# Optimization experiments

Measured on AMD Instinct MI355X. Metric: run time of the kernel, lower is better.

The kernel has to match this reference:

```python
import jax, jax.numpy as jnp
import numpy as np

B, L, D = 2, 2048, 1024
H = 16
DH = D // H
FACTOR = 0.6
U = max(1, min(L, int(FACTOR * L)))  # 1228 selected queries


def setup_inputs() -> dict:
    key = jax.random.key(0)
    ks = jax.random.split(key, 9)
    s = 0.02
    return {
        "x": jax.random.normal(ks[0], (B, L, D), dtype=jnp.float32),
        "Wq": jax.random.normal(ks[1], (D, D), dtype=jnp.float32) * s,
        "bq": jnp.zeros((D,), dtype=jnp.float32),
        "Wk": jax.random.normal(ks[2], (D, D), dtype=jnp.float32) * s,
        "bk": jnp.zeros((D,), dtype=jnp.float32),
        "Wv": jax.random.normal(ks[3], (D, D), dtype=jnp.float32) * s,
        "bv": jnp.zeros((D,), dtype=jnp.float32),
        "Wo": jax.random.normal(ks[4], (D, D), dtype=jnp.float32) * s,
        "bo": jnp.zeros((D,), dtype=jnp.float32),
    }


def _split_heads(x):
    b, l, d = x.shape
    return x.reshape(b, l, H, DH).transpose(0, 2, 1, 3)  # [b,h,l,dh]


def reference(x, Wq, bq, Wk, bk, Wv, bv, Wo, bo):
    b, l, _ = x.shape
    scale = 1.0 / jnp.sqrt(jnp.asarray(DH, dtype=x.dtype))

    q = _split_heads(x @ Wq + bq)  # [b,h,l,dh]
    k = _split_heads(x @ Wk + bk)
    v = _split_heads(x @ Wv + bv)

    # full scores for sparsity heuristic
    scores = jnp.einsum("bhqd,bhkd->bhqk", q, k) * scale  # [b,h,l,l]
    sparsity = scores.max(axis=-1) - scores.mean(axis=-1)  # [b,h,l]

    _, top_idx = jax.lax.top_k(sparsity, U)  # [b,h,U]

    # gather selected queries, attend only on those rows
    q_sel = jnp.take_along_axis(q, top_idx[..., None], axis=2)  # [b,h,U,dh]
    scores_sel = jnp.einsum("bhud,bhkd->bhuk", q_sel, k) * scale  # [b,h,U,l]
    attn = jax.nn.softmax(scores_sel, axis=-1)
    out_sel = jnp.einsum("bhuk,bhkd->bhud", attn, v)  # [b,h,U,dh]

    # scatter back into zero-initialized output
    bi = jnp.arange(b)[:, None, None]
    hi = jnp.arange(H)[None, :, None]
    out = jnp.zeros_like(q).at[bi, hi, top_idx].set(out_sel)  # [b,h,l,dh]

    out = out.transpose(0, 2, 1, 3).reshape(b, l, D)
    return out @ Wo + bo
```

## Files before the change

kernel.cpp:

```cpp
#include <hip/hip_runtime.h>
#include <math.h>
#include <stdint.h>

#define Bn 2
#define Ln 2048
#define Dn 1024
#define Hn 16
#define DHn 64
#define Un 1228
#define BHn (Bn*Hn)
#define SCALE 0.125f
#define WIN 32
#define WHALF 16
#define SXf 16.0f
#define SWf 256.0f
#define SQf 16.0f
#define SVf 16.0f
#define SPf 16.0f
#define ESC_PROJ (1.0f / 4096.0f)
#define ESC_OUT  (1.0f / 65536.0f)
#define PSC (SCALE / 256.0f)
#define QPS 88

typedef _Float16 f16;
typedef __attribute__((ext_vector_type(8))) _Float16 f16x8;
typedef __attribute__((ext_vector_type(4))) float f32x4;
struct h4s { f16 x, y, z, w; };

__device__ __forceinline__ void splitf16(float f, f16& hi, f16& lo) {
  hi = (f16)f;
  lo = (f16)(f - (float)hi);
}

__device__ __forceinline__ void gl_lds16(const void* g, void* l) {
  __builtin_amdgcn_global_load_lds(
      (const __attribute__((address_space(1))) void*)g,
      (__attribute__((address_space(3))) void*)l, 16, 0, 0);
}

#define MFMA(a, b, c) __builtin_amdgcn_mfma_f32_16x16x32_f16((a), (b), (c), 0, 0, 0)

__global__ __launch_bounds__(256) void split_kernel(
    const float* __restrict__ in, f16* __restrict__ oh, f16* __restrict__ ol, int n4) {
  int i = blockIdx.x * 256 + threadIdx.x;
  if (i >= n4) return;
  float4 v = ((const float4*)in)[i];
  h4s h, l;
  splitf16(v.x * SXf, h.x, l.x); splitf16(v.y * SXf, h.y, l.y);
  splitf16(v.z * SXf, h.z, l.z); splitf16(v.w * SXf, h.w, l.w);
  ((h4s*)oh)[i] = h; ((h4s*)ol)[i] = l;
}

__global__ __launch_bounds__(256) void tsplit_w4(
    const float* __restrict__ W0, const float* __restrict__ W1,
    const float* __restrict__ W2, const float* __restrict__ W3,
    f16* __restrict__ oh, f16* __restrict__ ol) {
  __shared__ float ts[64][65];
  const int t = threadIdx.x;
  const int r0 = blockIdx.x * 64, c0 = blockIdx.y * 64;
  const int z = blockIdx.z;
  const float* in = (z == 0) ? W0 : (z == 1) ? W1 : (z == 2) ? W2 : W3;
#pragma unroll
  for (int c = 0; c < 4; ++c) {
    int f = (c * 256 + t) * 4; int row = f >> 6, col = f & 63;
    float4 v = *(const float4*)&in[(size_t)(r0 + row) * Dn + c0 + col];
    ts[row][col] = v.x; ts[row][col + 1] = v.y; ts[row][col + 2] = v.z; ts[row][col + 3] = v.w;
  }
  __syncthreads();
#pragma unroll
  for (int c = 0; c < 4; ++c) {
    int f = (c * 256 + t) * 4; int crow = f >> 6, rcol = f & 63;
    h4s h, l;
    splitf16(ts[rcol + 0][crow] * SWf, h.x, l.x);
    splitf16(ts[rcol + 1][crow] * SWf, h.y, l.y);
    splitf16(ts[rcol + 2][crow] * SWf, h.z, l.z);
    splitf16(ts[rcol + 3][crow] * SWf, h.w, l.w);
    size_t o = (size_t)(z * 1024 + c0 + crow) * Dn + r0 + rcol;
    *(h4s*)&oh[o] = h; *(h4s*)&ol[o] = l;
  }
}

__global__ void gemm_qkv(
    const f16* __restrict__ Ah, const f16* __restrict__ Al,
    const f16* __restrict__ Bth, const f16* __restrict__ Btl,
    const float* __restrict__ bq, const float* __restrict__ bk, const float* __restrict__ bv,
    f16* __restrict__ Qbh, f16* __restrict__ Qbl,
    f16* __restrict__ Kbh, f16* __restrict__ Kbl,
    f16* __restrict__ Vh16, int K) {
  __shared__ f16 sAh[128 * 32], sAl[128 * 32], sBh[128 * 32], sBl[128 * 32];
  const int t = threadIdx.x;
  const int w = t >> 6, lane = t & 63, lm = lane & 15, q = lane >> 4;
  const int wr = w >> 1, wc = w & 1;
  const int n0 = blockIdx.x * 128, m0 = blockIdx.y * 128;
  f32x4 acc[4][4] = {};
  for (int k0 = 0; k0 < K; k0 += 32) {
    const f16* s0 = Ah + (size_t)m0 * K + k0;
    const f16* s1 = Al + (size_t)m0 * K + k0;
    const f16* s2 = Bth + (size_t)n0 * K + k0;
    const f16* s3 = Btl + (size_t)n0 * K + k0;
#pragma unroll
    for (int c = 0; c < 2; ++c) {
      int f = (c * 256 + t) * 8; int row = f >> 5, col = f & 31;
      size_t go = (size_t)row * K + col;
      gl_lds16(s0 + go, &sAh[f]);
      gl_lds16(s1 + go, &sAl[f]);
      gl_lds16(s2 + go, &sBh[f]);
      gl_lds16(s3 + go, &sBl[f]);
    }
    __syncthreads();
    f16x8 a_h[4], a_l[4], b_h[4], b_l[4];
#pragma unroll
    for (int mi = 0; mi < 4; ++mi) {
      int r = (wr * 64 + mi * 16 + lm) * 32 + q * 8;
      a_h[mi] = *(const f16x8*)&sAh[r];
      a_l[mi] = *(const f16x8*)&sAl[r];
    }
#pragma unroll
    for (int ni = 0; ni < 4; ++ni) {
      int r = (wc * 64 + ni * 16 + lm) * 32 + q * 8;
      b_h[ni] = *(const f16x8*)&sBh[r];
      b_l[ni] = *(const f16x8*)&sBl[r];
    }
#pragma unroll
    for (int mi = 0; mi < 4; ++mi)
#pragma unroll
      for (int ni = 0; ni < 4; ++ni) {
        acc[mi][ni] = MFMA(a_h[mi], b_h[ni], acc[mi][ni]);
        acc[mi][ni] = MFMA(a_h[mi], b_l[ni], acc[mi][ni]);
        acc[mi][ni] = MFMA(a_l[mi], b_h[ni], acc[mi][ni]);
      }
    __syncthreads();
  }
#pragma unroll
  for (int mi = 0; mi < 4; ++mi)
#pragma unroll
    for (int ni = 0; ni < 4; ++ni) {
      int nglob = n0 + wc * 64 + ni * 16;
      int seg = nglob >> 10;
      int c = (nglob & 1023) + lm;
      const float* bp = (seg == 0) ? bq : (seg == 1) ? bk : bv;
      float bvv = bp[c];
#pragma unroll
      for (int r = 0; r < 4; ++r) {
        int grow = m0 + wr * 64 + mi * 16 + q * 4 + r;
        float v = acc[mi][ni][r] * ESC_PROJ + bvv;
        size_t o = (size_t)grow * 1024 + c;
        if (seg == 0) {
          f16 hh, ll; splitf16(v * SQf, hh, ll); Qbh[o] = hh; Qbl[o] = ll;
        } else if (seg == 1) {
          f16 hh, ll; splitf16(v * SQf, hh, ll); Kbh[o] = hh; Kbl[o] = ll;
        } else {
          Vh16[o] = (f16)(v * SVf);
        }
      }
    }
}

__global__ __launch_bounds__(256) void tsplit_v(
    const f16* __restrict__ Vh16, f16* __restrict__ out) {
  __shared__ f16 ts[64][72];
  const int t = threadIdx.x;
  const int l0 = blockIdx.x * 64;
  const int bh = blockIdx.y, b = bh >> 4, h = bh & 15;
#pragma unroll
  for (int c = 0; c < 2; ++c) {
    int e = c * 256 + t; int row = e >> 3, cg = e & 7;
    *(uint4*)&ts[row][cg * 8] =
        *(const uint4*)&Vh16[((size_t)b * Ln + l0 + row) * Dn + h * DHn + cg * 8];
  }
  __syncthreads();
#pragma unroll
  for (int c = 0; c < 2; ++c) {
    int e = c * 256 + t; int drow = e >> 3, lg = e & 7;
    f16 tmp[8];
#pragma unroll
    for (int j = 0; j < 8; ++j) tmp[j] = ts[lg * 8 + j][drow];
    *(uint4*)&out[((size_t)bh * DHn + drow) * Ln + l0 + lg * 8] = *(uint4*)tmp;
  }
}

#define A1_STAGE_TILE(BUF, KOFF) do { \
    const f16* s0_ = A + (size_t)m0 * K + (KOFF); \
    const f16* s2_ = Bth + (size_t)n0 * K + (KOFF); \
    const f16* s3_ = Btl + (size_t)n0 * K + (KOFF); \
    _Pragma("unroll") for (int c_ = 0; c_ < 2; ++c_) { \
      int f_ = (c_ * 256 + t) * 8; int row_ = f_ >> 5, col_ = f_ & 31; \
      gl_lds16(s0_ + (size_t)row_ * K + col_, &sA[BUF][f_]); \
    } \
    { int f_ = t * 8; int row_ = f_ >> 5, col_ = f_ & 31; \
      gl_lds16(s2_ + (size_t)row_ * K + col_, &sBh[BUF][f_]); \
      gl_lds16(s3_ + (size_t)row_ * K + col_, &sBl[BUF][f_]); } } while (0)

__global__ __launch_bounds__(256, 4) void gemm_a1(
    const f16* __restrict__ A,
    const f16* __restrict__ Bth, const f16* __restrict__ Btl,
    const float* __restrict__ bias, float escale,
    float* __restrict__ Cf, int M, int N, int K) {
  __shared__ f16 sA[2][128 * 32], sBh[2][64 * 32], sBl[2][64 * 32];
  const int t = threadIdx.x;
  const int w = t >> 6, lane = t & 63, lm = lane & 15, q = lane >> 4;
  const int wr = w >> 1, wc = w & 1;
  int ob = blockIdx.x;
  int wg = (ob & 7) * 64 + (ob >> 3);
  const int n0 = (wg & 15) * 64, m0 = (wg >> 4) * 128;
  f32x4 acc[4][2] = {};
  A1_STAGE_TILE(0, 0);
  asm volatile("s_waitcnt vmcnt(0)" ::: "memory");
  __builtin_amdgcn_s_barrier();
  for (int k0 = 0; k0 < K; k0 += 32) {
    const int cur = (k0 >> 5) & 1;
    if (k0 + 32 < K) A1_STAGE_TILE(cur ^ 1, k0 + 32);
    f16x8 a_[4], b_h[2], b_l[2];
#pragma unroll
    for (int mi = 0; mi < 4; ++mi)
      a_[mi] = *(const f16x8*)&sA[cur][(wr * 64 + mi * 16 + lm) * 32 + q * 8];
#pragma unroll
    for (int ni = 0; ni < 2; ++ni) {
      int r = (wc * 32 + ni * 16 + lm) * 32 + q * 8;
      b_h[ni] = *(const f16x8*)&sBh[cur][r];
      b_l[ni] = *(const f16x8*)&sBl[cur][r];
    }
#pragma unroll
    for (int mi = 0; mi < 4; ++mi)
#pragma unroll
      for (int ni = 0; ni < 2; ++ni) {
        acc[mi][ni] = MFMA(a_[mi], b_h[ni], acc[mi][ni]);
        acc[mi][ni] = MFMA(a_[mi], b_l[ni], acc[mi][ni]);
      }
    asm volatile("s_waitcnt vmcnt(0) lgkmcnt(0)" ::: "memory");
    __builtin_amdgcn_s_barrier();
  }
#pragma unroll
  for (int mi = 0; mi < 4; ++mi)
#pragma unroll
    for (int ni = 0; ni < 2; ++ni) {
      int gcol = n0 + wc * 32 + ni * 16 + lm;
      float bvv = bias[gcol];
#pragma unroll
      for (int r = 0; r < 4; ++r) {
        int grow = m0 + wr * 64 + mi * 16 + q * 4 + r;
        Cf[(size_t)grow * N + gcol] = acc[mi][ni][r] * escale + bvv;
      }
    }
}

__global__ __launch_bounds__(256) void ksum_part(
    const f16* __restrict__ Kh, float* __restrict__ ksum) {
  __shared__ float red[4][64];
  const int t = threadIdx.x, d = t & 63, seg = t >> 6;
  const int bx = blockIdx.x, bh = blockIdx.y, b = bh >> 4, h = bh & 15;
  float s = 0.f;
  const int lbase = bx * 256 + seg * 64;
  for (int r = 0; r < 64; ++r) {
    size_t o = ((size_t)b * Ln + lbase + r) * Dn + h * DHn + d;
    s += (float)Kh[o];
  }
  red[seg][d] = s;
  __syncthreads();
  if (t < 64) atomicAdd(&ksum[bh * DHn + t], red[0][t] + red[1][t] + red[2][t] + red[3][t]);
}

__global__ __launch_bounds__(256, 2) void attn_stats_mfma(
    const f16* __restrict__ Qh, const f16* __restrict__ Kh,
    const float* __restrict__ ksum,
    float* __restrict__ row_max, float* __restrict__ spars) {
  __shared__ f16 sQh[128 * 64], sKh[128 * 64];
  __shared__ float redm[128][5];
  const int t = threadIdx.x;
  const int w = t >> 6, lane = t & 63, lm = lane & 15, q = lane >> 4;
  const int bh = blockIdx.y, b = bh >> 4, h = bh & 15;
  const int q0 = blockIdx.x * 128;
  const f16* qsh = Qh + ((size_t)b * Ln + q0) * Dn + h * DHn;
#pragma unroll
  for (int c = 0; c < 4; ++c) {
    int f = (c * 256 + t) * 8; int row = f >> 6, c16 = (f >> 3) & 7;
    size_t go = (size_t)row * Dn + ((c16 ^ (row & 7)) << 3);
    gl_lds16(qsh + go, &sQh[f]);
  }
  __syncthreads();
  f16x8 a_h[8][2];
#pragma unroll
  for (int mi = 0; mi < 8; ++mi)
#pragma unroll
    for (int ks = 0; ks < 2; ++ks) {
      int row = mi * 16 + lm;
      int r = row * 64 + (((ks * 4 + q) ^ (row & 7)) << 3);
      a_h[mi][ks] = *(const f16x8*)&sQh[r];
    }
  float rmax[8][4];
#pragma unroll
  for (int mi = 0; mi < 8; ++mi)
#pragma unroll
    for (int r = 0; r < 4; ++r) rmax[mi][r] = -1e30f;

  for (int kt = 0; kt < Ln / 128; ++kt) {
    __syncthreads();
    const f16* ksh = Kh + ((size_t)b * Ln + kt * 128) * Dn + h * DHn;
#pragma unroll
    for (int c = 0; c < 4; ++c) {
      int f = (c * 256 + t) * 8; int row = f >> 6, c16 = (f >> 3) & 7;
      size_t go = (size_t)row * Dn + ((c16 ^ (row & 7)) << 3);
      gl_lds16(ksh + go, &sKh[f]);
    }
    __syncthreads();
#pragma unroll
    for (int ni = 0; ni < 2; ++ni) {
      int bcol = (w * 2 + ni) * 16;
      f16x8 b_h[2];
#pragma unroll
      for (int ks = 0; ks < 2; ++ks) {
        int row = bcol + lm;
        int r = row * 64 + (((ks * 4 + q) ^ (row & 7)) << 3);
        b_h[ks] = *(const f16x8*)&sKh[r];
      }
#pragma unroll
      for (int mi = 0; mi < 8; ++mi) {
        f32x4 acc = {0.f, 0.f, 0.f, 0.f};
        __builtin_amdgcn_s_setprio(1);
        acc = MFMA(a_h[mi][0], b_h[0], acc);
        acc = MFMA(a_h[mi][1], b_h[1], acc);
        __builtin_amdgcn_s_setprio(0);
#pragma unroll
        for (int r = 0; r < 4; ++r) rmax[mi][r] = fmaxf(rmax[mi][r], acc[r]);
      }
    }
  }
#pragma unroll
  for (int mi = 0; mi < 8; ++mi)
#pragma unroll
    for (int r = 0; r < 4; ++r) {
      float v = rmax[mi][r];
      v = fmaxf(v, __shfl_xor(v, 1)); v = fmaxf(v, __shfl_xor(v, 2));
      v = fmaxf(v, __shfl_xor(v, 4)); v = fmaxf(v, __shfl_xor(v, 8));
      if (lm == 0) redm[mi * 16 + q * 4 + r][w] = v;
    }
  __syncthreads();
  if (t < 128) {
    float m = fmaxf(fmaxf(redm[t][0], redm[t][1]), fmaxf(redm[t][2], redm[t][3]));
    float dot = 0.f;
    const float* kp = ksum + bh * DHn;
#pragma unroll
    for (int d = 0; d < 64; ++d) {
      int idx = t * 64 + ((((d >> 3) ^ (t & 7)) << 3) | (d & 7));
      dot += (float)sQh[idx] * kp[d];
    }
    row_max[(size_t)bh * Ln + q0 + t] = m * PSC;
    spars[(size_t)bh * Ln + q0 + t] = m * PSC - dot * (PSC / (float)Ln);
  }
}

__global__ __launch_bounds__(1024) void topk_sort(
    const float* __restrict__ spars, int* __restrict__ top_idx, int* __restrict__ wrow) {
  __shared__ unsigned long long keys[Ln];
  const int t = threadIdx.x;
  const int bh = blockIdx.x;
  for (int i = t; i < Ln; i += 1024) {
    unsigned u = __float_as_uint(spars[(size_t)bh * Ln + i]);
    u = (u & 0x80000000u) ? ~u : (u | 0x80000000u);
    u = ~u;
    keys[i] = ((unsigned long long)u << 32) | (unsigned)i;
  }
  __syncthreads();
  for (int k = 2; k <= Ln; k <<= 1) {
    for (int j = k >> 1; j > 0; j >>= 1) {
      int i = ((t & ~(j - 1)) << 1) | (t & (j - 1));
      int ixj = i | j;
      unsigned long long a = keys[i], bb = keys[ixj];
      bool up = ((i & k) == 0);
      if ((a > bb) == up) { keys[i] = bb; keys[ixj] = a; }
      __syncthreads();
    }
  }
  for (int u = t; u < Un - WHALF; u += 1024)
    top_idx[(size_t)bh * Un + u] = (int)(keys[u] & 0xFFFFFFFFu);
  if (t < WIN) wrow[bh * WIN + t] = (int)(keys[Un - WHALF + t] & 0xFFFFFFFFu);
}

__global__ __launch_bounds__(256) void refine_part(
    const f16* __restrict__ Qbh, const f16* __restrict__ Qbl,
    const f16* __restrict__ Kbh, const f16* __restrict__ Kbl,
    const int* __restrict__ wrow,
    float* __restrict__ pmaxf, float* __restrict__ psum) {
  __shared__ float qs[WIN][68];
  __shared__ float redm[4][WIN], reds[4][WIN];
  const int t = threadIdx.x;
  const int bx = blockIdx.x, bh = blockIdx.y, b = bh >> 4, h = bh & 15;
  {
    int j = t >> 3, d0 = (t & 7) * 8;
    int qi = wrow[bh * WIN + j];
    size_t o = ((size_t)b * Ln + qi) * Dn + h * DHn + d0;
    f16x8 vh = *(const f16x8*)&Qbh[o];
    f16x8 vl = *(const f16x8*)&Qbl[o];
#pragma unroll
    for (int e = 0; e < 8; ++e) qs[j][d0 + e] = (float)vh[e] + (float)vl[e];
  }
  __syncthreads();
  const int ki = bx * 256 + t;
  const size_t ko = ((size_t)b * Ln + ki) * Dn + h * DHn;
  float s[WIN];
#pragma unroll
  for (int j = 0; j < WIN; ++j) s[j] = 0.f;
  for (int d0 = 0; d0 < 64; d0 += 8) {
    f16x8 vh = *(const f16x8*)&Kbh[ko + d0];
    f16x8 vl = *(const f16x8*)&Kbl[ko + d0];
    float kf[8];
#pragma unroll
    for (int e = 0; e < 8; ++e) kf[e] = (float)vh[e] + (float)vl[e];
#pragma unroll
    for (int e = 0; e < 8; ++e)
#pragma unroll
      for (int j = 0; j < WIN; ++j)
        s[j] = fmaf(kf[e], qs[j][d0 + e], s[j]);
  }
  const int w = t >> 6, lane = t & 63;
#pragma unroll
  for (int j = 0; j < WIN; ++j) {
    float mx = s[j], sm = s[j];
#pragma unroll
    for (int off = 1; off < 64; off <<= 1) {
      mx = fmaxf(mx, __shfl_xor(mx, off));
      sm += __shfl_xor(sm, off);
    }
    if (lane == 0) { redm[w][j] = mx; reds[w][j] = sm; }
  }
  __syncthreads();
  if (t < WIN) {
    float mx = fmaxf(fmaxf(redm[0][t], redm[1][t]), fmaxf(redm[2][t], redm[3][t]));
    float sm = reds[0][t] + reds[1][t] + reds[2][t] + reds[3][t];
    size_t o = ((size_t)bh * WIN + t) * 8 + bx;
    pmaxf[o] = mx;
    psum[o] = sm;
  }
}

__global__ __launch_bounds__(64) void topk_final(
    const float* __restrict__ pmaxf, const float* __restrict__ psum,
    const int* __restrict__ wrow, int* __restrict__ top_idx) {
  __shared__ float spxL[WIN];
  const int bh = blockIdx.x;
  const int t = threadIdx.x;
  if (t < WIN) {
    float m = -1e30f, s = 0.f;
#pragma unroll
    for (int p = 0; p < 8; ++p) {
      size_t o = ((size_t)bh * WIN + t) * 8 + p;
      m = fmaxf(m, pmaxf[o]);
      s += psum[o];
    }
    spxL[t] = PSC * (m - s * (1.0f / (float)Ln));
  }
  __syncthreads();
  if (t != 0) return;
  float v[WIN]; int r[WIN];
#pragma unroll
  for (int j = 0; j < WIN; ++j) { v[j] = spxL[j]; r[j] = wrow[bh * WIN + j]; }
  unsigned taken = 0;
  for (int s2 = 0; s2 < WHALF; ++s2) {
    int best = -1;
    for (int j = 0; j < WIN; ++j) {
      if (taken & (1u << j)) continue;
      if (best < 0 || v[j] > v[best] || (v[j] == v[best] && r[j] < r[best])) best = j;
    }
    taken |= 1u << best;
    top_idx[(size_t)bh * Un + (Un - WHALF) + s2] = r[best];
  }
}

__global__ __launch_bounds__(256, 3) void attn_sel_part(
    const f16* __restrict__ Qh, const f16* __restrict__ Kh,
    const f16* __restrict__ Vth,
    const int* __restrict__ topi, const float* __restrict__ row_max,
    float* __restrict__ pO, float* __restrict__ pD) {
  __shared__ f16 sK[2][64 * 64], sV[2][64 * 64];
  __shared__ f16 sQP[64 * QPS];
  __shared__ float rmL[64];
  __shared__ int qxL[64];
  __shared__ float dred[64][5];
  const int t = threadIdx.x;
  const int w = t >> 6, lane = t & 63, lm = lane & 15, q = lane >> 4;
  const int half = blockIdx.y & 1, bh = blockIdx.y >> 1, b = bh >> 4, h = bh & 15;
  const int u0 = blockIdx.x * 64;
  const int nrows = (Un - u0 < 64) ? (Un - u0) : 64;
  if (t < 64) {
    int qi = topi[(size_t)bh * Un + ((t < nrows) ? (u0 + t) : 0)];
    qxL[t] = qi;
    rmL[t] = row_max[(size_t)bh * Ln + qi];
  }
  __syncthreads();
#pragma unroll
  for (int c = 0; c < 2; ++c) {
    int f = (c * 256 + t) * 8; int row = f >> 6, col = f & 63;
    size_t go = ((size_t)b * Ln + qxL[row]) * Dn + h * DHn + col;
    *(uint4*)&sQP[row * QPS + col] = *(const uint4*)&Qh[go];
  }
  __syncthreads();
  f16x8 aq[4][2];
#pragma unroll
  for (int mi = 0; mi < 4; ++mi)
#pragma unroll
    for (int ks = 0; ks < 2; ++ks)
      aq[mi][ks] = *(const f16x8*)&sQP[(mi * 16 + lm) * QPS + ks * 32 + q * 8];
  f32x4 oacc[4] = {};
  float dacc[4][4] = {};

  const f16* kbase = Kh + (size_t)b * Ln * Dn + h * DHn;
  const f16* vbase = Vth + (size_t)bh * DHn * Ln;

  {
    const int l0 = half * 1024;
#pragma unroll
    for (int c = 0; c < 2; ++c) {
      int f = (c * 256 + t) * 8; int row = f >> 6, c16 = (f >> 3) & 7;
      int sc = (c16 ^ (row & 7)) << 3;
      gl_lds16(kbase + (size_t)(l0 + row) * Dn + sc, &sK[0][f]);
      gl_lds16(vbase + (size_t)row * Ln + l0 + sc, &sV[0][f]);
    }
  }
  asm volatile("s_waitcnt vmcnt(0) lgkmcnt(0)" ::: "memory");
  __builtin_amdgcn_s_barrier();

  for (int kt = 0; kt < 16; ++kt) {
    const int cur = kt & 1;
    f16x8 kb[2];
#pragma unroll
    for (int ks = 0; ks < 2; ++ks) {
      int row = w * 16 + lm;
      kb[ks] = *(const f16x8*)&sK[cur][row * 64 + (((ks * 4 + q) ^ (row & 7)) << 3)];
    }
    if (kt < 15) {
      const int ln0 = half * 1024 + (kt + 1) * 64;
#pragma unroll
      for (int c = 0; c < 2; ++c) {
        int f = (c * 256 + t) * 8; int row = f >> 6, c16 = (f >> 3) & 7;
        int sc = (c16 ^ (row & 7)) << 3;
        gl_lds16(kbase + (size_t)(ln0 + row) * Dn + sc, &sK[cur ^ 1][f]);
        gl_lds16(vbase + (size_t)row * Ln + ln0 + sc, &sV[cur ^ 1][f]);
      }
    }
#pragma unroll
    for (int mi = 0; mi < 4; ++mi) {
      f32x4 acc = {0.f, 0.f, 0.f, 0.f};
      __builtin_amdgcn_s_setprio(1);
      acc = MFMA(aq[mi][0], kb[0], acc);
      acc = MFMA(aq[mi][1], kb[1], acc);
      __builtin_amdgcn_s_setprio(0);
#pragma unroll
      for (int r = 0; r < 4; ++r) {
        int row = mi * 16 + q * 4 + r;
        float p = __expf(acc[r] * PSC - rmL[row]);
        dacc[mi][r] += p;
        sQP[row * QPS + w * 16 + lm] = (f16)(p * SPf);
      }
    }
    asm volatile("s_waitcnt lgkmcnt(0)" ::: "memory");
    __builtin_amdgcn_s_barrier();
    f16x8 vb[2];
#pragma unroll
    for (int ks = 0; ks < 2; ++ks) {
      int row = w * 16 + lm;
      vb[ks] = *(const f16x8*)&sV[cur][row * 64 + (((ks * 4 + q) ^ (row & 7)) << 3)];
    }
#pragma unroll
    for (int mi = 0; mi < 4; ++mi) {
      f16x8 pf0 = *(const f16x8*)&sQP[(mi * 16 + lm) * QPS + 0 * 32 + q * 8];
      f16x8 pf1 = *(const f16x8*)&sQP[(mi * 16 + lm) * QPS + 1 * 32 + q * 8];
      __builtin_amdgcn_s_setprio(1);
      oacc[mi] = MFMA(pf0, vb[0], oacc[mi]);
      oacc[mi] = MFMA(pf1, vb[1], oacc[mi]);
      __builtin_amdgcn_s_setprio(0);
    }
    asm volatile("s_waitcnt vmcnt(0)" ::: "memory");
    __builtin_amdgcn_s_barrier();
  }
#pragma unroll
  for (int mi = 0; mi < 4; ++mi)
#pragma unroll
    for (int r = 0; r < 4; ++r) {
      float v = dacc[mi][r];
      v += __shfl_xor(v, 1); v += __shfl_xor(v, 2);
      v += __shfl_xor(v, 4); v += __shfl_xor(v, 8);
      if (lm == 0) dred[mi * 16 + q * 4 + r][w] = v;
    }
  __syncthreads();
  const size_t pbase = ((size_t)half * BHn + bh) * 1280 + u0;
  if (t < 64)
    pD[pbase + t] = dred[t][0] + dred[t][1] + dred[t][2] + dred[t][3];
#pragma unroll
  for (int mi = 0; mi < 4; ++mi)
#pragma unroll
    for (int r = 0; r < 4; ++r) {
      int row = mi * 16 + q * 4 + r;
      pO[(pbase + row) * 64 + w * 16 + lm] = oacc[mi][r];
    }
}

__global__ __launch_bounds__(256) void attn_combine(
    const float* __restrict__ pO, const float* __restrict__ pD,
    const int* __restrict__ topi, f16* __restrict__ AOh) {
  const int t = threadIdx.x;
  const int u0 = blockIdx.x * 64, bh = blockIdx.y, b = bh >> 4, h = bh & 15;
  const int nrows = (Un - u0 < 64) ? (Un - u0) : 64;
  const int row = t >> 2, pg = t & 3;
  if (row >= nrows) return;
  int qi = topi[(size_t)bh * Un + u0 + row];
  size_t i0 = (size_t)bh * 1280 + u0 + row;
  size_t i1 = (size_t)BHn * 1280 + i0;
  float dinv = 1.0f / (pD[i0] + pD[i1]);
  const float* p0 = &pO[i0 * 64 + pg * 16];
  const float* p1 = &pO[i1 * 64 + pg * 16];
  f16 buf[16];
#pragma unroll
  for (int c = 0; c < 4; ++c) {
    float4 a = *(const float4*)&p0[c * 4];
    float4 bb = *(const float4*)&p1[c * 4];
    buf[c * 4 + 0] = (f16)((a.x + bb.x) * dinv);
    buf[c * 4 + 1] = (f16)((a.y + bb.y) * dinv);
    buf[c * 4 + 2] = (f16)((a.z + bb.z) * dinv);
    buf[c * 4 + 3] = (f16)((a.w + bb.w) * dinv);
  }
  f16* dst = &AOh[((size_t)b * Ln + qi) * Dn + h * DHn + pg * 16];
  *(uint4*)&dst[0] = *(uint4*)&buf[0];
  *(uint4*)&dst[8] = *(uint4*)&buf[8];
}

extern "C" void kernel_launch(void* const* d_in, const int* in_sizes, int n_in,
                              void* d_out, int out_size, void* d_ws, size_t ws_size,
                              hipStream_t stream) {
  (void)in_sizes; (void)n_in; (void)out_size; (void)ws_size;
  const float* x  = (const float*)d_in[0];
  const float* Wq = (const float*)d_in[1];
  const float* bq = (const float*)d_in[2];
  const float* Wk = (const float*)d_in[3];
  const float* bk = (const float*)d_in[4];
  const float* Wv = (const float*)d_in[5];
  const float* bv = (const float*)d_in[6];
  const float* Wo = (const float*)d_in[7];
  const float* bo = (const float*)d_in[8];
  float* out = (float*)d_out;

  uint8_t* p = (uint8_t*)d_ws;
  const size_t NE = (size_t)Bn * Ln * Dn;
  f16* xh = (f16*)p;  p += NE * 2;
  f16* xl = (f16*)p;  p += NE * 2;
  f16* Wt_h = (f16*)p; p += (size_t)4096 * Dn * 2;
  f16* Wt_l = (f16*)p; p += (size_t)4096 * Dn * 2;
  f16* Qbh = (f16*)p; p += NE * 2;
  f16* Qbl = (f16*)p; p += NE * 2;
  f16* Kbh = (f16*)p; p += NE * 2;
  f16* Kbl = (f16*)p; p += NE * 2;
  f16* Vh16 = (f16*)p; p += NE * 2;
  f16* Vth  = (f16*)p; p += NE * 2;
  float* rowmax = (float*)p; p += (size_t)BHn * Ln * 4;
  float* spars  = (float*)p; p += (size_t)BHn * Ln * 4;
  float* ksum   = (float*)p; p += (size_t)BHn * DHn * 4;
  int* topi     = (int*)p;   p += (size_t)BHn * Un * 4;
  int* wrow     = (int*)p;   p += (size_t)BHn * WIN * 4;
  float* pmaxf  = (float*)p; p += (size_t)BHn * WIN * 8 * 4;
  float* psum   = (float*)p; p += (size_t)BHn * WIN * 8 * 4;
  float* pD     = (float*)p; p += (size_t)2 * BHn * 1280 * 4;
  float* pO     = (float*)p; p += (size_t)2 * BHn * 1280 * 64 * 4;
  f16* AOh = xh;

  dim3 blk(256);
  hipLaunchKernelGGL(split_kernel, dim3((int)(NE / 4 / 256)), blk, 0, stream, x, xh, xl, (int)(NE / 4));
  hipLaunchKernelGGL(tsplit_w4, dim3(16, 16, 4), blk, 0, stream, Wq, Wk, Wv, Wo, Wt_h, Wt_l);
  hipLaunchKernelGGL(gemm_qkv, dim3(24, 32), blk, 0, stream, xh, xl, Wt_h, Wt_l,
                     bq, bk, bv, Qbh, Qbl, Kbh, Kbl, Vh16, Dn);
  hipLaunchKernelGGL(tsplit_v, dim3(Ln / 64, BHn), blk, 0, stream, Vh16, Vth);
  hipMemsetAsync(ksum, 0, (size_t)BHn * DHn * 4, stream);
  hipLaunchKernelGGL(ksum_part, dim3(8, BHn), blk, 0, stream, Kbh, ksum);
  hipLaunchKernelGGL(attn_stats_mfma, dim3(Ln / 128, BHn), blk, 0, stream,
                     Qbh, Kbh, ksum, rowmax, spars);
  hipLaunchKernelGGL(topk_sort, dim3(BHn), dim3(1024), 0, stream, spars, topi, wrow);
  hipLaunchKernelGGL(refine_part, dim3(8, BHn), blk, 0, stream,
                     Qbh, Qbl, Kbh, Kbl, wrow, pmaxf, psum);
  hipLaunchKernelGGL(topk_final, dim3(BHn), dim3(64), 0, stream, pmaxf, psum, wrow, topi);
  hipMemsetAsync(AOh, 0, NE * 2, stream);
  hipLaunchKernelGGL(attn_sel_part, dim3((Un + 63) / 64, 2 * BHn), blk, 0, stream,
                     Qbh, Kbh, Vth, topi, rowmax, pO, pD);
  hipLaunchKernelGGL(attn_combine, dim3((Un + 63) / 64, BHn), blk, 0, stream,
                     pO, pD, topi, AOh);
  hipLaunchKernelGGL(gemm_a1, dim3(512), blk, 0, stream, AOh,
                     Wt_h + (size_t)3072 * Dn, Wt_l + (size_t)3072 * Dn, bo,
                     ESC_OUT, out, Bn * Ln, Dn, Dn);
}
```

Measured before the change: 375.1 us.

## Fuse prep kernels, merge V-transpose with ksum, drop split-K attention combine

Merges the x split and the weight transpose-split into one launch, and the V transpose and K-sum into another, using block-index ranges to pick the work. The selected-query attention kernel no longer splits the key range in two halves with a separate combine pass. Each block now loops over all 32 key tiles and writes normalized f16 output straight into the scattered AO buffer. This removes launches and the fp32 partial-output round trip, but the attention grid is halved, so there is less parallelism and each block runs a longer serial loop.

```diff
diff --git a/kernel.cpp b/kernel.cpp
--- a/kernel.cpp
+++ b/kernel.cpp
@@ -40,25 +40,26 @@
 
 #define MFMA(a, b, c) __builtin_amdgcn_mfma_f32_16x16x32_f16((a), (b), (c), 0, 0, 0)
 
-__global__ __launch_bounds__(256) void split_kernel(
-    const float* __restrict__ in, f16* __restrict__ oh, f16* __restrict__ ol, int n4) {
-  int i = blockIdx.x * 256 + threadIdx.x;
-  if (i >= n4) return;
-  float4 v = ((const float4*)in)[i];
-  h4s h, l;
-  splitf16(v.x * SXf, h.x, l.x); splitf16(v.y * SXf, h.y, l.y);
-  splitf16(v.z * SXf, h.z, l.z); splitf16(v.w * SXf, h.w, l.w);
-  ((h4s*)oh)[i] = h; ((h4s*)ol)[i] = l;
-}
-
-__global__ __launch_bounds__(256) void tsplit_w4(
+__global__ __launch_bounds__(256) void prep_fused(
+    const float* __restrict__ x, f16* __restrict__ xh, f16* __restrict__ xl, int n4,
     const float* __restrict__ W0, const float* __restrict__ W1,
     const float* __restrict__ W2, const float* __restrict__ W3,
     f16* __restrict__ oh, f16* __restrict__ ol) {
   __shared__ float ts[64][65];
   const int t = threadIdx.x;
-  const int r0 = blockIdx.x * 64, c0 = blockIdx.y * 64;
-  const int z = blockIdx.z;
+  const int bid = blockIdx.x;
+  if (bid < 4096) {
+    int i = bid * 256 + t;
+    if (i >= n4) return;
+    float4 v = ((const float4*)x)[i];
+    h4s h, l;
+    splitf16(v.x * SXf, h.x, l.x); splitf16(v.y * SXf, h.y, l.y);
+    splitf16(v.z * SXf, h.z, l.z); splitf16(v.w * SXf, h.w, l.w);
+    ((h4s*)xh)[i] = h; ((h4s*)xl)[i] = l;
+    return;
+  }
+  const int r = bid - 4096;
+  const int r0 = (r & 15) * 64, c0 = ((r >> 4) & 15) * 64, z = r >> 8;
   const float* in = (z == 0) ? W0 : (z == 1) ? W1 : (z == 2) ? W2 : W3;
 #pragma unroll
   for (int c = 0; c < 4; ++c) {
@@ -156,27 +157,45 @@
     }
 }
 
-__global__ __launch_bounds__(256) void tsplit_v(
-    const f16* __restrict__ Vh16, f16* __restrict__ out) {
+__global__ __launch_bounds__(256) void vk_fused(
+    const f16* __restrict__ Vh16, f16* __restrict__ out,
+    const f16* __restrict__ Kh, float* __restrict__ ksum) {
   __shared__ f16 ts[64][72];
-  const int t = threadIdx.x;
-  const int l0 = blockIdx.x * 64;
-  const int bh = blockIdx.y, b = bh >> 4, h = bh & 15;
-#pragma unroll
-  for (int c = 0; c < 2; ++c) {
-    int e = c * 256 + t; int row = e >> 3, cg = e & 7;
-    *(uint4*)&ts[row][cg * 8] =
-        *(const uint4*)&Vh16[((size_t)b * Ln + l0 + row) * Dn + h * DHn + cg * 8];
-  }
-  __syncthreads();
-#pragma unroll
-  for (int c = 0; c < 2; ++c) {
-    int e = c * 256 + t; int drow = e >> 3, lg = e & 7;
-    f16 tmp[8];
-#pragma unroll
-    for (int j = 0; j < 8; ++j) tmp[j] = ts[lg * 8 + j][drow];
-    *(uint4*)&out[((size_t)bh * DHn + drow) * Ln + l0 + lg * 8] = *(uint4*)tmp;
-  }
+  __shared__ float red[4][64];
+  const int t = threadIdx.x;
+  const int bid = blockIdx.x;
+  if (bid < 1024) {
+    const int l0 = (bid & 31) * 64;
+    const int bh = bid >> 5, b = bh >> 4, h = bh & 15;
+#pragma unroll
+    for (int c = 0; c < 2; ++c) {
+      int e = c * 256 + t; int row = e >> 3, cg = e & 7;
+      *(uint4*)&ts[row][cg * 8] =
+          *(const uint4*)&Vh16[((size_t)b * Ln + l0 + row) * Dn + h * DHn + cg * 8];
+    }
+    __syncthreads();
+#pragma unroll
+    for (int c = 0; c < 2; ++c) {
+      int e = c * 256 + t; int drow = e >> 3, lg = e & 7;
+      f16 tmp[8];
+#pragma unroll
+      for (int j = 0; j < 8; ++j) tmp[j] = ts[lg * 8 + j][drow];
+      *(uint4*)&out[((size_t)bh * DHn + drow) * Ln + l0 + lg * 8] = *(uint4*)tmp;
+    }
+    return;
+  }
+  const int r0 = bid - 1024;
+  const int bx = r0 & 7, bh = r0 >> 3, b = bh >> 4, h = bh & 15;
+  const int d = t & 63, seg = t >> 6;
+  float s = 0.f;
+  const int lbase = bx * 256 + seg * 64;
+  for (int r = 0; r < 64; ++r) {
+    size_t o = ((size_t)b * Ln + lbase + r) * Dn + h * DHn + d;
+    s += (float)Kh[o];
+  }
+  red[seg][d] = s;
+  __syncthreads();
+  if (t < 64) atomicAdd(&ksum[bh * DHn + t], red[0][t] + red[1][t] + red[2][t] + red[3][t]);
 }
 
 #define A1_STAGE_TILE(BUF, KOFF) do { \
@@ -244,22 +263,6 @@
     }
 }
 
-__global__ __launch_bounds__(256) void ksum_part(
-    const f16* __restrict__ Kh, float* __restrict__ ksum) {
-  __shared__ float red[4][64];
-  const int t = threadIdx.x, d = t & 63, seg = t >> 6;
-  const int bx = blockIdx.x, bh = blockIdx.y, b = bh >> 4, h = bh & 15;
-  float s = 0.f;
-  const int lbase = bx * 256 + seg * 64;
-  for (int r = 0; r < 64; ++r) {
-    size_t o = ((size_t)b * Ln + lbase + r) * Dn + h * DHn + d;
-    s += (float)Kh[o];
-  }
-  red[seg][d] = s;
-  __syncthreads();
-  if (t < 64) atomicAdd(&ksum[bh * DHn + t], red[0][t] + red[1][t] + red[2][t] + red[3][t]);
-}
-
 __global__ __launch_bounds__(256, 2) void attn_stats_mfma(
     const f16* __restrict__ Qh, const f16* __restrict__ Kh,
     const float* __restrict__ ksum,
@@ -466,11 +469,11 @@
   }
 }
 
-__global__ __launch_bounds__(256, 3) void attn_sel_part(
+__global__ __launch_bounds__(256, 3) void attn_sel(
     const f16* __restrict__ Qh, const f16* __restrict__ Kh,
     const f16* __restrict__ Vth,
     const int* __restrict__ topi, const float* __restrict__ row_max,
-    float* __restrict__ pO, float* __restrict__ pD) {
+    f16* __restrict__ AOh) {
   __shared__ f16 sK[2][64 * 64], sV[2][64 * 64];
   __shared__ f16 sQP[64 * QPS];
   __shared__ float rmL[64];
@@ -478,7 +481,7 @@
   __shared__ float dred[64][5];
   const int t = threadIdx.x;
   const int w = t >> 6, lane = t & 63, lm = lane & 15, q = lane >> 4;
-  const int half = blockIdx.y & 1, bh = blockIdx.y >> 1, b = bh >> 4, h = bh & 15;
+  const int bh = blockIdx.y, b = bh >> 4, h = bh & 15;
   const int u0 = blockIdx.x * 64;
   const int nrows = (Un - u0 < 64) ? (Un - u0) : 64;
   if (t < 64) {
@@ -506,20 +509,17 @@
   const f16* kbase = Kh + (size_t)b * Ln * Dn + h * DHn;
   const f16* vbase = Vth + (size_t)bh * DHn * Ln;
 
-  {
-    const int l0 = half * 1024;
-#pragma unroll
-    for (int c = 0; c < 2; ++c) {
-      int f = (c * 256 + t) * 8; int row = f >> 6, c16 = (f >> 3) & 7;
-      int sc = (c16 ^ (row & 7)) << 3;
-      gl_lds16(kbase + (size_t)(l0 + row) * Dn + sc, &sK[0][f]);
-      gl_lds16(vbase + (size_t)row * Ln + l0 + sc, &sV[0][f]);
-    }
+#pragma unroll
+  for (int c = 0; c < 2; ++c) {
+    int f = (c * 256 + t) * 8; int row = f >> 6, c16 = (f >> 3) & 7;
+    int sc = (c16 ^ (row & 7)) << 3;
+    gl_lds16(kbase + (size_t)row * Dn + sc, &sK[0][f]);
+    gl_lds16(vbase + (size_t)row * Ln + sc, &sV[0][f]);
   }
   asm volatile("s_waitcnt vmcnt(0) lgkmcnt(0)" ::: "memory");
   __builtin_amdgcn_s_barrier();
 
-  for (int kt = 0; kt < 16; ++kt) {
+  for (int kt = 0; kt < 32; ++kt) {
     const int cur = kt & 1;
     f16x8 kb[2];
 #pragma unroll
@@ -527,8 +527,8 @@
       int row = w * 16 + lm;
       kb[ks] = *(const f16x8*)&sK[cur][row * 64 + (((ks * 4 + q) ^ (row & 7)) << 3)];
     }
-    if (kt < 15) {
-      const int ln0 = half * 1024 + (kt + 1) * 64;
+    if (kt < 31) {
+      const int ln0 = (kt + 1) * 64;
 #pragma unroll
       for (int c = 0; c < 2; ++c) {
         int f = (c * 256 + t) * 8; int row = f >> 6, c16 = (f >> 3) & 7;
@@ -582,45 +582,17 @@
       if (lm == 0) dred[mi * 16 + q * 4 + r][w] = v;
     }
   __syncthreads();
-  const size_t pbase = ((size_t)half * BHn + bh) * 1280 + u0;
-  if (t < 64)
-    pD[pbase + t] = dred[t][0] + dred[t][1] + dred[t][2] + dred[t][3];
 #pragma unroll
   for (int mi = 0; mi < 4; ++mi)
 #pragma unroll
     for (int r = 0; r < 4; ++r) {
       int row = mi * 16 + q * 4 + r;
-      pO[(pbase + row) * 64 + w * 16 + lm] = oacc[mi][r];
-    }
-}
-
-__global__ __launch_bounds__(256) void attn_combine(
-    const float* __restrict__ pO, const float* __restrict__ pD,
-    const int* __restrict__ topi, f16* __restrict__ AOh) {
-  const int t = threadIdx.x;
-  const int u0 = blockIdx.x * 64, bh = blockIdx.y, b = bh >> 4, h = bh & 15;
-  const int nrows = (Un - u0 < 64) ? (Un - u0) : 64;
-  const int row = t >> 2, pg = t & 3;
-  if (row >= nrows) return;
-  int qi = topi[(size_t)bh * Un + u0 + row];
-  size_t i0 = (size_t)bh * 1280 + u0 + row;
-  size_t i1 = (size_t)BHn * 1280 + i0;
-  float dinv = 1.0f / (pD[i0] + pD[i1]);
-  const float* p0 = &pO[i0 * 64 + pg * 16];
-  const float* p1 = &pO[i1 * 64 + pg * 16];
-  f16 buf[16];
-#pragma unroll
-  for (int c = 0; c < 4; ++c) {
-    float4 a = *(const float4*)&p0[c * 4];
-    float4 bb = *(const float4*)&p1[c * 4];
-    buf[c * 4 + 0] = (f16)((a.x + bb.x) * dinv);
-    buf[c * 4 + 1] = (f16)((a.y + bb.y) * dinv);
-    buf[c * 4 + 2] = (f16)((a.z + bb.z) * dinv);
-    buf[c * 4 + 3] = (f16)((a.w + bb.w) * dinv);
-  }
-  f16* dst = &AOh[((size_t)b * Ln + qi) * Dn + h * DHn + pg * 16];
-  *(uint4*)&dst[0] = *(uint4*)&buf[0];
-  *(uint4*)&dst[8] = *(uint4*)&buf[8];
+      if (row < nrows) {
+        float dinv = 1.0f / (dred[row][0] + dred[row][1] + dred[row][2] + dred[row][3]);
+        AOh[((size_t)b * Ln + qxL[row]) * Dn + h * DHn + w * 16 + lm] =
+            (f16)(oacc[mi][r] * dinv);
+      }
+    }
 }
 
 extern "C" void kernel_launch(void* const* d_in, const int* in_sizes, int n_in,
@@ -657,18 +629,15 @@
   int* wrow     = (int*)p;   p += (size_t)BHn * WIN * 4;
   float* pmaxf  = (float*)p; p += (size_t)BHn * WIN * 8 * 4;
   float* psum   = (float*)p; p += (size_t)BHn * WIN * 8 * 4;
-  float* pD     = (float*)p; p += (size_t)2 * BHn * 1280 * 4;
-  float* pO     = (float*)p; p += (size_t)2 * BHn * 1280 * 64 * 4;
   f16* AOh = xh;
 
   dim3 blk(256);
-  hipLaunchKernelGGL(split_kernel, dim3((int)(NE / 4 / 256)), blk, 0, stream, x, xh, xl, (int)(NE / 4));
-  hipLaunchKernelGGL(tsplit_w4, dim3(16, 16, 4), blk, 0, stream, Wq, Wk, Wv, Wo, Wt_h, Wt_l);
+  hipLaunchKernelGGL(prep_fused, dim3(4096 + 1024), blk, 0, stream,
+                     x, xh, xl, (int)(NE / 4), Wq, Wk, Wv, Wo, Wt_h, Wt_l);
   hipLaunchKernelGGL(gemm_qkv, dim3(24, 32), blk, 0, stream, xh, xl, Wt_h, Wt_l,
                      bq, bk, bv, Qbh, Qbl, Kbh, Kbl, Vh16, Dn);
-  hipLaunchKernelGGL(tsplit_v, dim3(Ln / 64, BHn), blk, 0, stream, Vh16, Vth);
   hipMemsetAsync(ksum, 0, (size_t)BHn * DHn * 4, stream);
-  hipLaunchKernelGGL(ksum_part, dim3(8, BHn), blk, 0, stream, Kbh, ksum);
+  hipLaunchKernelGGL(vk_fused, dim3(1024 + 256), blk, 0, stream, Vh16, Vth, Kbh, ksum);
   hipLaunchKernelGGL(attn_stats_mfma, dim3(Ln / 128, BHn), blk, 0, stream,
                      Qbh, Kbh, ksum, rowmax, spars);
   hipLaunchKernelGGL(topk_sort, dim3(BHn), dim3(1024), 0, stream, spars, topi, wrow);
@@ -676,10 +645,8 @@
                      Qbh, Qbl, Kbh, Kbl, wrow, pmaxf, psum);
   hipLaunchKernelGGL(topk_final, dim3(BHn), dim3(64), 0, stream, pmaxf, psum, wrow, topi);
   hipMemsetAsync(AOh, 0, NE * 2, stream);
-  hipLaunchKernelGGL(attn_sel_part, dim3((Un + 63) / 64, 2 * BHn), blk, 0, stream,
-                     Qbh, Kbh, Vth, topi, rowmax, pO, pD);
-  hipLaunchKernelGGL(attn_combine, dim3((Un + 63) / 64, BHn), blk, 0, stream,
-                     pO, pD, topi, AOh);
+  hipLaunchKernelGGL(attn_sel, dim3((Un + 63) / 64, BHn), blk, 0, stream,
+                     Qbh, Kbh, Vth, topi, rowmax, AOh);
   hipLaunchKernelGGL(gemm_a1, dim3(512), blk, 0, stream, AOh,
                      Wt_h + (size_t)3072 * Dn, Wt_l + (size_t)3072 * Dn, bo,
                      ESC_OUT, out, Bn * Ln, Dn, Dn);
```

Measured after the change: 377.3 us. About the same (+0.6%).
